# Optimization experiments

Hardware: AMD Instinct MI355X
Metric: run time of the kernel (lower is better)

The kernel has to match this reference:

```python
import jax, jax.numpy as jnp
import numpy as np

NUM_HEADS = 16
WINDOW = 64


def setup_inputs() -> dict:
    key = jax.random.key(0)
    ks = jax.random.split(key, 6)
    b, l, d = 2, 2048, 1024
    s = 1.0 / np.sqrt(d)
    return {
        "x": jax.random.normal(ks[0], (b, l, d), dtype=jnp.float32),
        "Wq": jax.random.normal(ks[1], (d, d), dtype=jnp.float32) * s,
        "Wk": jax.random.normal(ks[2], (d, d), dtype=jnp.float32) * s,
        "Wv": jax.random.normal(ks[3], (d, d), dtype=jnp.float32) * s,
        "Wo": jax.random.normal(ks[4], (d, d), dtype=jnp.float32) * s,
        "bo": jax.random.normal(ks[5], (d,), dtype=jnp.float32) * 0.01,
    }


def reference(x, Wq, Wk, Wv, Wo, bo):
    b, l, d = x.shape
    h, w = NUM_HEADS, WINDOW
    dh = d // h
    p = w // 2
    # Projections. Padding is zeros and proj_k/proj_v have no bias, so
    # padding-then-projecting equals projecting-then-zero-padding.
    q = (x @ Wq.T).reshape(b, l, h, dh)                     # (b,l,h,dh)
    xp = jnp.pad(x, ((0, 0), (p, p), (0, 0)))               # (b,l+2p,d)
    k = (xp @ Wk.T).reshape(b, l + 2 * p, h, dh)
    v = (xp @ Wv.T).reshape(b, l + 2 * p, h, dh)
    # Sliding windows: query i attends to padded positions i .. i+w-1
    win_idx = jnp.arange(l)[:, None] + jnp.arange(w)[None, :]  # (l,w)
    kw = k[:, win_idx]                                       # (b,l,w,h,dh)
    vw = v[:, win_idx]                                       # (b,l,w,h,dh)
    scale = 1.0 / np.float32(np.sqrt(dh))
    scores = jnp.einsum('blhd,blwhd->blhw', q, kw) * scale   # (b,l,h,w)
    attn = jax.nn.softmax(scores, axis=-1)
    out = jnp.einsum('blhw,blwhd->blhd', attn, vw).reshape(b, l, d)
    return out @ Wo.T + bo
```

## Files before the change

kernel.cpp:

```cpp
#include <hip/hip_runtime.h>
#include <hip/hip_bf16.h>
#include <cstdint>

typedef __bf16 bf16;
typedef __bf16 bf16x4 __attribute__((ext_vector_type(4)));
typedef __bf16 bf16x8 __attribute__((ext_vector_type(8)));
typedef float floatx4 __attribute__((ext_vector_type(4)));

typedef __attribute__((address_space(1))) void as1_void;
typedef __attribute__((address_space(3))) void as3_void;

__device__ __forceinline__ void gld16(const void* g, void* l) {
#if __has_builtin(__builtin_amdgcn_global_load_lds)
  __builtin_amdgcn_global_load_lds((as1_void*)(uintptr_t)g, (as3_void*)l, 16, 0, 0);
#else
  *(uint4*)l = *(const uint4*)g;
#endif
}

__global__ __launch_bounds__(256) void convert_kernel(
    const float* __restrict__ x, const float* __restrict__ wq,
    const float* __restrict__ wk, const float* __restrict__ wv,
    const float* __restrict__ wo, bf16* __restrict__ xbf,
    bf16* __restrict__ wqkv, bf16* __restrict__ wob) {
  int i = blockIdx.x * 256 + threadIdx.x;
  const float* src;
  bf16* dst;
  int off;
  if (i < 1048576) {
    src = x; dst = xbf; off = i;
  } else if (i < 1310720) {
    src = wq; dst = wqkv; off = i - 1048576;
  } else if (i < 1572864) {
    src = wk; dst = wqkv + 1048576; off = i - 1310720;
  } else if (i < 1835008) {
    src = wv; dst = wqkv + 2097152; off = i - 1572864;
  } else {
    src = wo; dst = wob; off = i - 1835008;
  }
  float4 v = ((const float4*)src)[off];
  bf16x4 o;
  o[0] = (bf16)v.x; o[1] = (bf16)v.y; o[2] = (bf16)v.z; o[3] = (bf16)v.w;
  ((bf16x4*)dst)[off] = o;
}

template <int MODE, int BN>
__global__ __launch_bounds__(256) void gemm_nt(const bf16* __restrict__ A,
                                               const bf16* __restrict__ Bm,
                                               bf16* __restrict__ Cb,
                                               float* __restrict__ Cf,
                                               const float* __restrict__ bias,
                                               int M, int N, int K) {
  constexpr int WN = BN / 2;
  constexpr int NI = WN / 16;
  __shared__ __attribute__((aligned(16))) bf16 As[128 * 32];
  __shared__ __attribute__((aligned(16))) bf16 Bs[BN * 32];
  const int tid = threadIdx.x;
  const int lane = tid & 63;
  const int wave = tid >> 6;
  const int quad = lane >> 4;
  const int n0 = lane & 15;
  const int wm = wave >> 1;
  const int wn = wave & 1;
  const int nwg = gridDim.x * gridDim.y;
  const int nid = blockIdx.y * gridDim.x + blockIdx.x;
  int sid = nid;
  if ((nwg & 7) == 0) sid = (nid & 7) * (nwg >> 3) + (nid >> 3);
  const int bN = sid % gridDim.x, bM = sid / gridDim.x;
  const bf16* Ab = A + (size_t)bM * 128 * K;
  const bf16* Bb = Bm + (size_t)bN * BN * K;
  const int c0 = tid, c1 = tid + 256;
  floatx4 acc[4][NI] = {};
  for (int k0 = 0; k0 < K; k0 += 32) {
    gld16(Ab + (size_t)(c0 >> 2) * K + k0 + (c0 & 3) * 8, &As[c0 * 8]);
    gld16(Ab + (size_t)(c1 >> 2) * K + k0 + (c1 & 3) * 8, &As[c1 * 8]);
#pragma unroll
    for (int cc = 0; cc < BN * 4; cc += 256) {
      const int c = cc + tid;
      gld16(Bb + (size_t)(c >> 2) * K + k0 + (c & 3) * 8, &Bs[c * 8]);
    }
    __syncthreads();
    bf16x8 af[4], bfr[NI];
#pragma unroll
    for (int mi = 0; mi < 4; ++mi)
      af[mi] = *(const bf16x8*)&As[(wm * 64 + mi * 16 + n0) * 32 + quad * 8];
#pragma unroll
    for (int ni = 0; ni < NI; ++ni)
      bfr[ni] = *(const bf16x8*)&Bs[(wn * WN + ni * 16 + n0) * 32 + quad * 8];
#pragma unroll
    for (int mi = 0; mi < 4; ++mi)
#pragma unroll
      for (int ni = 0; ni < NI; ++ni)
        acc[mi][ni] = __builtin_amdgcn_mfma_f32_16x16x32_bf16(
            af[mi], bfr[ni], acc[mi][ni], 0, 0, 0);
    __syncthreads();
  }
  const int rowBase = bM * 128 + wm * 64;
  const int colBase = bN * BN + wn * WN;
#pragma unroll
  for (int ni = 0; ni < NI; ++ni) {
    const int col = colBase + ni * 16 + n0;
    float badd = 0.f;
    if (MODE == 1) badd = bias[col];
#pragma unroll
    for (int mi = 0; mi < 4; ++mi)
#pragma unroll
      for (int r = 0; r < 4; ++r) {
        const int row = rowBase + mi * 16 + quad * 4 + r;
        if (MODE == 0)
          Cb[(size_t)row * N + col] = (bf16)acc[mi][ni][r];
        else
          Cf[(size_t)row * N + col] = acc[mi][ni][r] + badd;
      }
  }
}

#define BAR asm volatile("s_barrier" ::: "memory")
#define LGKM0                                         \
  do {                                                \
    asm volatile("s_waitcnt lgkmcnt(0)" ::: "memory");\
    __builtin_amdgcn_sched_barrier(0);                \
  } while (0)

#define STAGE(buf, op, h, t)                                                   \
  do {                                                                         \
    const char* g_ = ((op) ? Bb : Ab) + (size_t)(h) * 128 * Kb +               \
                     (size_t)(t) * 128 + rowOff;                               \
    char* l_ = lds + (buf) * 65536 + (op) * 32768 + (h) * 16384 + tid * 16;    \
    gld16(g_, l_);                                                             \
    gld16(g_ + 64 * Kb, l_ + 8192);                                            \
  } while (0)

#define LDA(buf, mh)                                                           \
  do {                                                                         \
    _Pragma("unroll") for (int q = 0; q < 4; ++q)                              \
      _Pragma("unroll") for (int ks = 0; ks < 2; ++ks)                         \
        aR[q][ks] = *(const bf16x8*)(lds + (buf) * 65536 + wm * 16384 +        \
            ((mh) * 64 + q * 16 + n0) * 128 + ((ks * 64 + quad * 16) ^ swz));  \
  } while (0)

#define LDB(buf, g)                                                            \
  do {                                                                         \
    _Pragma("unroll") for (int j = 0; j < 2; ++j)                              \
      _Pragma("unroll") for (int ks = 0; ks < 2; ++ks) {                       \
        const int row_ = wn * 64 + ((g) * 2 + j) * 16 + n0;                    \
        bR[g][j][ks] = *(const bf16x8*)(lds + (buf) * 65536 + 32768 +          \
            (row_ >> 7) * 16384 + (row_ & 127) * 128 +                         \
            ((ks * 64 + quad * 16) ^ swz));                                    \
      }                                                                        \
  } while (0)

#define MM(mh, nh)                                                             \
  do {                                                                         \
    __builtin_amdgcn_s_setprio(1);                                             \
    _Pragma("unroll") for (int q = 0; q < 4; ++q)                              \
      _Pragma("unroll") for (int j = 0; j < 2; ++j)                            \
        _Pragma("unroll") for (int ks = 0; ks < 2; ++ks)                       \
          acc[(mh) * 4 + q][(nh) * 2 + j] =                                    \
              __builtin_amdgcn_mfma_f32_16x16x32_bf16(                         \
                  aR[q][ks], bR[nh][j][ks],                                    \
                  acc[(mh) * 4 + q][(nh) * 2 + j], 0, 0, 0);                   \
    __builtin_amdgcn_s_setprio(0);                                             \
  } while (0)

__global__ __launch_bounds__(512, 2) void gemm256_nt(
    const bf16* __restrict__ A, const bf16* __restrict__ Bm,
    bf16* __restrict__ C, int M, int N, int K) {
  __shared__ __attribute__((aligned(16))) char lds[131072];
  const int tid = threadIdx.x;
  const int lane = tid & 63, wave = tid >> 6;
  const int quad = lane >> 4, n0 = lane & 15;
  const int wm = wave >> 2, wn = wave & 3;
  const int swz = (n0 & 7) << 4;
  const size_t Kb = (size_t)K * 2;
  const char* Ab = (const char*)(A + (size_t)blockIdx.y * 256 * K);
  const char* Bb = (const char*)(Bm + (size_t)blockIdx.x * 256 * K);
  const int srow = tid >> 3;
  const size_t rowOff = (size_t)srow * Kb + (size_t)(16 * ((tid & 7) ^ (srow & 7)));

  floatx4 acc[8][4] = {};
  bf16x8 aR[4][2];
  bf16x8 bR[2][2][2];

  const int NT = K >> 6;
  const int NI = K >> 7;

  STAGE(0, 0, 0, 0); STAGE(0, 0, 1, 0); STAGE(0, 1, 0, 0); STAGE(0, 1, 1, 0);
  STAGE(1, 1, 0, 1); STAGE(1, 0, 0, 1);
  asm volatile("s_waitcnt vmcnt(4)" ::: "memory");
  BAR;

  for (int i = 0; i < NI; ++i) {
    const int T = 2 * i;
    const bool s2 = (T + 2 < NT), s3 = (T + 3 < NT);
    LDB(0, 0); LDA(0, 0);
    STAGE(1, 0, 1, T + 1);
    BAR; LGKM0; MM(0, 0); BAR;
    LDB(0, 1);
    STAGE(1, 1, 1, T + 1);
    BAR; LGKM0; MM(0, 1); BAR;
    LDA(0, 1);
    if (s2) STAGE(0, 1, 0, T + 2);
    BAR; LGKM0; MM(1, 0); BAR;
    if (s2) STAGE(0, 1, 1, T + 2);
    BAR; MM(1, 1);
    if (i + 1 < NI) { asm volatile("s_waitcnt vmcnt(4)" ::: "memory"); }
    else           { asm volatile("s_waitcnt vmcnt(0)" ::: "memory"); }
    BAR;
    LDB(1, 0); LDA(1, 0);
    if (s2) STAGE(0, 0, 0, T + 2);
    BAR; LGKM0; MM(0, 0); BAR;
    LDB(1, 1);
    if (s2) STAGE(0, 0, 1, T + 2);
    BAR; LGKM0; MM(0, 1); BAR;
    LDA(1, 1);
    if (s3) STAGE(1, 1, 0, T + 3);
    BAR; LGKM0; MM(1, 0); BAR;
    if (s3) STAGE(1, 0, 0, T + 3);
    BAR; MM(1, 1);
    asm volatile("s_waitcnt vmcnt(4)" ::: "memory");
    BAR;
  }

  const int rowBase = blockIdx.y * 256 + wm * 128 + quad * 4;
  const int colBase = blockIdx.x * 256 + wn * 64 + n0;
#pragma unroll
  for (int mi = 0; mi < 8; ++mi)
#pragma unroll
    for (int ni = 0; ni < 4; ++ni)
#pragma unroll
      for (int r = 0; r < 4; ++r)
        C[(size_t)(rowBase + mi * 16 + r) * N + colBase + ni * 16] =
            (bf16)acc[mi][ni][r];
}

#undef BAR
#undef LGKM0
#undef STAGE
#undef LDA
#undef LDB
#undef MM

__global__ __launch_bounds__(256) void attn_kernel(const bf16* __restrict__ qkv,
                                                   bf16* __restrict__ aout) {
  __shared__ __attribute__((aligned(16))) bf16 Ks[128 * 72];
  __shared__ __attribute__((aligned(16))) bf16 VsPs[128 * 72];
  __shared__ __attribute__((aligned(16))) bf16 Vt[64 * 136];
  const int bid = blockIdx.x;
  const int b = bid >> 9;
  const int h = (bid >> 5) & 15;
  const int i0 = (bid & 31) * 64;
  const int tid = threadIdx.x;
  const int wave = tid >> 6, lane = tid & 63;
  const int quad = lane >> 4, n0 = lane & 15;
  bf16* Vs = VsPs;

  bf16x8 aq[2];
#pragma unroll
  for (int ks = 0; ks < 2; ++ks)
    aq[ks] = *(const bf16x8*)(qkv +
        (size_t)(b * 2048 + i0 + wave * 16 + n0) * 3072 + h * 64 + ks * 32 + quad * 8);

#pragma unroll
  for (int it = 0; it < 4; ++it) {
    const int idx = it * 256 + tid;
    const int r = idx >> 3, c = idx & 7;
    const int j = i0 - 32 + r;
    uint4 kv_ = make_uint4(0u, 0u, 0u, 0u);
    uint4 vv = make_uint4(0u, 0u, 0u, 0u);
    if (j >= 0 && j < 2048) {
      const bf16* base = qkv + (size_t)(b * 2048 + j) * 3072 + 1024 + h * 64 + c * 8;
      kv_ = *(const uint4*)base;
      vv = *(const uint4*)(base + 1024);
    }
    *(uint4*)&Ks[r * 72 + c * 8] = kv_;
    *(uint4*)&Vs[r * 72 + c * 8] = vv;
  }
  __syncthreads();

#pragma unroll
  for (int it = 0; it < 4; ++it) {
    const int idx = it * 256 + tid;
    const int t = idx & 127, c = idx >> 7;
    bf16x8 v = *(const bf16x8*)&Vs[t * 72 + c * 8];
#pragma unroll
    for (int jj = 0; jj < 8; ++jj) Vt[(c * 8 + jj) * 136 + t] = v[jj];
  }
  __syncthreads();

  floatx4 accS[8] = {};
#pragma unroll
  for (int nt = 0; nt < 8; ++nt)
#pragma unroll
    for (int ks = 0; ks < 2; ++ks) {
      bf16x8 bk = *(const bf16x8*)&Ks[(nt * 16 + n0) * 72 + ks * 32 + quad * 8];
      accS[nt] = __builtin_amdgcn_mfma_f32_16x16x32_bf16(aq[ks], bk, accS[nt], 0, 0, 0);
    }

  float mrow[4] = {-1e30f, -1e30f, -1e30f, -1e30f};
#pragma unroll
  for (int nt = 0; nt < 8; ++nt)
#pragma unroll
    for (int r = 0; r < 4; ++r) {
      const int q64 = wave * 16 + quad * 4 + r;
      const int t = nt * 16 + n0;
      float s = accS[nt][r] * 0.125f;
      if (t < q64 || t >= q64 + 64) s = -1e30f;
      accS[nt][r] = s;
      mrow[r] = fmaxf(mrow[r], s);
    }
#pragma unroll
  for (int off = 1; off < 16; off <<= 1)
#pragma unroll
    for (int r = 0; r < 4; ++r)
      mrow[r] = fmaxf(mrow[r], __shfl_xor(mrow[r], off));
  float lrow[4] = {0.f, 0.f, 0.f, 0.f};
#pragma unroll
  for (int nt = 0; nt < 8; ++nt)
#pragma unroll
    for (int r = 0; r < 4; ++r) {
      const float e = __expf(accS[nt][r] - mrow[r]);
      accS[nt][r] = e;
      lrow[r] += e;
    }
#pragma unroll
  for (int off = 1; off < 16; off <<= 1)
#pragma unroll
    for (int r = 0; r < 4; ++r) lrow[r] += __shfl_xor(lrow[r], off);

  bf16* Pw = &VsPs[wave * 16 * 136];
#pragma unroll
  for (int r = 0; r < 4; ++r) {
    const float inv = 1.f / lrow[r];
#pragma unroll
    for (int nt = 0; nt < 8; ++nt)
      Pw[(quad * 4 + r) * 136 + nt * 16 + n0] = (bf16)(accS[nt][r] * inv);
  }

  floatx4 accO[4] = {};
#pragma unroll
  for (int kt = 0; kt < 4; ++kt) {
    bf16x8 ap = *(const bf16x8*)&Pw[n0 * 136 + kt * 32 + quad * 8];
#pragma unroll
    for (int dt = 0; dt < 4; ++dt) {
      bf16x8 bv = *(const bf16x8*)&Vt[(dt * 16 + n0) * 136 + kt * 32 + quad * 8];
      accO[dt] = __builtin_amdgcn_mfma_f32_16x16x32_bf16(ap, bv, accO[dt], 0, 0, 0);
    }
  }
#pragma unroll
  for (int dt = 0; dt < 4; ++dt)
#pragma unroll
    for (int r = 0; r < 4; ++r) {
      const int q64 = wave * 16 + quad * 4 + r;
      aout[(size_t)(b * 2048 + i0 + q64) * 1024 + h * 64 + dt * 16 + n0] =
          (bf16)accO[dt][r];
    }
}

extern "C" void kernel_launch(void* const* d_in, const int* in_sizes, int n_in,
                              void* d_out, int out_size, void* d_ws, size_t ws_size,
                              hipStream_t stream) {
  const float* x = (const float*)d_in[0];
  const float* wq = (const float*)d_in[1];
  const float* wk = (const float*)d_in[2];
  const float* wv = (const float*)d_in[3];
  const float* wo = (const float*)d_in[4];
  const float* bo = (const float*)d_in[5];
  char* ws = (char*)d_ws;
  bf16* xbf = (bf16*)(ws);
  bf16* wqkv = (bf16*)(ws + (8u << 20));
  bf16* wob = (bf16*)(ws + (14u << 20));
  bf16* qkv = (bf16*)(ws + (16u << 20));
  bf16* aout = xbf;

  convert_kernel<<<8192, 256, 0, stream>>>(x, wq, wk, wv, wo, xbf, wqkv, wob);
  gemm256_nt<<<dim3(12, 16), 512, 0, stream>>>(xbf, wqkv, qkv, 4096, 3072, 1024);
  attn_kernel<<<1024, 256, 0, stream>>>(qkv, aout);
  gemm_nt<1, 64><<<dim3(16, 32), 256, 0, stream>>>(aout, wob, nullptr,
                                                   (float*)d_out, bo, 4096, 1024,
                                                   1024);
}
```

Measured before the change: 154.5 us.

## Use 256x192 tiles in QKV GEMM to fill all CUs

The QKV projection GEMM tile changes from 256x256 to 256x192, so the grid grows from 192 to 256 blocks, one per CU on a 256-CU part, and the tail wave goes away. The LDS staging, fragment loads, MFMA groups and vmcnt waits are reworked to match the uneven 3-column B split per wave and the smaller LDS footprint. In exchange, arithmetic intensity per block drops and the pipeline schedule is less symmetric.

Result: faster. 151.3 us (-2.1%).

```diff
diff --git a/kernel.cpp b/kernel.cpp
--- a/kernel.cpp
+++ b/kernel.cpp
@@ -122,51 +122,56 @@
     __builtin_amdgcn_sched_barrier(0);                \
   } while (0)
 
-#define STAGE(buf, op, h, t)                                                   \
-  do {                                                                         \
-    const char* g_ = ((op) ? Bb : Ab) + (size_t)(h) * 128 * Kb +               \
-                     (size_t)(t) * 128 + rowOff;                               \
-    char* l_ = lds + (buf) * 65536 + (op) * 32768 + (h) * 16384 + tid * 16;    \
-    gld16(g_, l_);                                                             \
-    gld16(g_ + 64 * Kb, l_ + 8192);                                            \
-  } while (0)
-
-#define LDA(buf, mh)                                                           \
+#define STAGEU(buf, op, u, t)                                                  \
+  gld16(((op) ? Bb : Ab) + (size_t)(u) * 64 * Kb + (size_t)(t) * 128 + rowOff, \
+        lds + (buf) * 57344 + (op) * 32768 + (u) * 8192 + tid * 16)
+
+#define LDA_(buf, mh)                                                          \
   do {                                                                         \
     _Pragma("unroll") for (int q = 0; q < 4; ++q)                              \
       _Pragma("unroll") for (int ks = 0; ks < 2; ++ks)                         \
-        aR[q][ks] = *(const bf16x8*)(lds + (buf) * 65536 + wm * 16384 +        \
-            ((mh) * 64 + q * 16 + n0) * 128 + ((ks * 64 + quad * 16) ^ swz));  \
-  } while (0)
-
-#define LDB(buf, g)                                                            \
+        aR[q][ks] = *(const bf16x8*)(lds + (buf) * 57344 +                     \
+            (wm * 2 + (mh)) * 8192 + (q * 16 + n0) * 128 +                     \
+            ((ks * 64 + quad * 16) ^ swz));                                    \
+  } while (0)
+
+#define LDB_(buf, g)                                                           \
   do {                                                                         \
-    _Pragma("unroll") for (int j = 0; j < 2; ++j)                              \
+    _Pragma("unroll") for (int j = 0; j < ((g) ? 1 : 2); ++j)                  \
       _Pragma("unroll") for (int ks = 0; ks < 2; ++ks) {                       \
-        const int row_ = wn * 64 + ((g) * 2 + j) * 16 + n0;                    \
-        bR[g][j][ks] = *(const bf16x8*)(lds + (buf) * 65536 + 32768 +          \
-            (row_ >> 7) * 16384 + (row_ & 127) * 128 +                         \
+        const int ni_ = (g) ? 2 : j;                                           \
+        const int row_ = wn * 48 + ni_ * 16 + n0;                              \
+        bR[ni_][ks] = *(const bf16x8*)(lds + (buf) * 57344 + 32768 +           \
+            (row_ >> 6) * 8192 + (row_ & 63) * 128 +                           \
             ((ks * 64 + quad * 16) ^ swz));                                    \
       }                                                                        \
   } while (0)
 
-#define MM(mh, nh)                                                             \
+#define MMg0(mh)                                                               \
   do {                                                                         \
     __builtin_amdgcn_s_setprio(1);                                             \
     _Pragma("unroll") for (int q = 0; q < 4; ++q)                              \
       _Pragma("unroll") for (int j = 0; j < 2; ++j)                            \
         _Pragma("unroll") for (int ks = 0; ks < 2; ++ks)                       \
-          acc[(mh) * 4 + q][(nh) * 2 + j] =                                    \
-              __builtin_amdgcn_mfma_f32_16x16x32_bf16(                         \
-                  aR[q][ks], bR[nh][j][ks],                                    \
-                  acc[(mh) * 4 + q][(nh) * 2 + j], 0, 0, 0);                   \
+          acc[(mh) * 4 + q][j] = __builtin_amdgcn_mfma_f32_16x16x32_bf16(      \
+              aR[q][ks], bR[j][ks], acc[(mh) * 4 + q][j], 0, 0, 0);            \
     __builtin_amdgcn_s_setprio(0);                                             \
   } while (0)
 
-__global__ __launch_bounds__(512, 2) void gemm256_nt(
+#define MMg1(mh)                                                               \
+  do {                                                                         \
+    __builtin_amdgcn_s_setprio(1);                                             \
+    _Pragma("unroll") for (int q = 0; q < 4; ++q)                              \
+      _Pragma("unroll") for (int ks = 0; ks < 2; ++ks)                         \
+        acc[(mh) * 4 + q][2] = __builtin_amdgcn_mfma_f32_16x16x32_bf16(        \
+            aR[q][ks], bR[2][ks], acc[(mh) * 4 + q][2], 0, 0, 0);              \
+    __builtin_amdgcn_s_setprio(0);                                             \
+  } while (0)
+
+__global__ __launch_bounds__(512, 2) void gemm192_nt(
     const bf16* __restrict__ A, const bf16* __restrict__ Bm,
     bf16* __restrict__ C, int M, int N, int K) {
-  __shared__ __attribute__((aligned(16))) char lds[131072];
+  __shared__ __attribute__((aligned(16))) char lds[114688];
   const int tid = threadIdx.x;
   const int lane = tid & 63, wave = tid >> 6;
   const int quad = lane >> 4, n0 = lane & 15;
@@ -174,60 +179,63 @@
   const int swz = (n0 & 7) << 4;
   const size_t Kb = (size_t)K * 2;
   const char* Ab = (const char*)(A + (size_t)blockIdx.y * 256 * K);
-  const char* Bb = (const char*)(Bm + (size_t)blockIdx.x * 256 * K);
+  const char* Bb = (const char*)(Bm + (size_t)blockIdx.x * 192 * K);
   const int srow = tid >> 3;
   const size_t rowOff = (size_t)srow * Kb + (size_t)(16 * ((tid & 7) ^ (srow & 7)));
 
-  floatx4 acc[8][4] = {};
+  floatx4 acc[8][3] = {};
   bf16x8 aR[4][2];
-  bf16x8 bR[2][2][2];
+  bf16x8 bR[3][2];
 
   const int NT = K >> 6;
   const int NI = K >> 7;
 
-  STAGE(0, 0, 0, 0); STAGE(0, 0, 1, 0); STAGE(0, 1, 0, 0); STAGE(0, 1, 1, 0);
-  STAGE(1, 1, 0, 1); STAGE(1, 0, 0, 1);
-  asm volatile("s_waitcnt vmcnt(4)" ::: "memory");
+  STAGEU(0, 0, 0, 0); STAGEU(0, 0, 1, 0); STAGEU(0, 0, 2, 0); STAGEU(0, 0, 3, 0);
+  STAGEU(0, 1, 0, 0); STAGEU(0, 1, 1, 0); STAGEU(0, 1, 2, 0);
+  STAGEU(1, 1, 0, 1); STAGEU(1, 1, 1, 1); STAGEU(1, 1, 2, 1);
+  STAGEU(1, 0, 0, 1); STAGEU(1, 0, 2, 1);
+  asm volatile("s_waitcnt vmcnt(5)" ::: "memory");
   BAR;
 
   for (int i = 0; i < NI; ++i) {
     const int T = 2 * i;
-    const bool s2 = (T + 2 < NT), s3 = (T + 3 < NT);
-    LDB(0, 0); LDA(0, 0);
-    STAGE(1, 0, 1, T + 1);
-    BAR; LGKM0; MM(0, 0); BAR;
-    LDB(0, 1);
-    STAGE(1, 1, 1, T + 1);
-    BAR; LGKM0; MM(0, 1); BAR;
-    LDA(0, 1);
-    if (s2) STAGE(0, 1, 0, T + 2);
-    BAR; LGKM0; MM(1, 0); BAR;
-    if (s2) STAGE(0, 1, 1, T + 2);
-    BAR; MM(1, 1);
-    if (i + 1 < NI) { asm volatile("s_waitcnt vmcnt(4)" ::: "memory"); }
-    else           { asm volatile("s_waitcnt vmcnt(0)" ::: "memory"); }
+    const bool s2 = (T + 2 < NT);
+    LDB_(0, 0); LDA_(0, 0);
+    STAGEU(1, 0, 1, T + 1);
+    BAR; LGKM0; MMg0(0); BAR;
+    LDB_(0, 1);
+    STAGEU(1, 0, 3, T + 1);
+    BAR; LGKM0; MMg1(0); BAR;
+    LDA_(0, 1);
+    if (s2) { STAGEU(0, 1, 0, T + 2); STAGEU(0, 1, 1, T + 2); }
+    BAR; LGKM0; MMg0(1); BAR;
+    if (s2) STAGEU(0, 1, 2, T + 2);
+    BAR; MMg1(1);
+    if (i + 1 < NI) { asm volatile("s_waitcnt vmcnt(3)" ::: "memory"); }
+    else            { asm volatile("s_waitcnt vmcnt(0)" ::: "memory"); }
     BAR;
-    LDB(1, 0); LDA(1, 0);
-    if (s2) STAGE(0, 0, 0, T + 2);
-    BAR; LGKM0; MM(0, 0); BAR;
-    LDB(1, 1);
-    if (s2) STAGE(0, 0, 1, T + 2);
-    BAR; LGKM0; MM(0, 1); BAR;
-    LDA(1, 1);
-    if (s3) STAGE(1, 1, 0, T + 3);
-    BAR; LGKM0; MM(1, 0); BAR;
-    if (s3) STAGE(1, 0, 0, T + 3);
-    BAR; MM(1, 1);
-    asm volatile("s_waitcnt vmcnt(4)" ::: "memory");
+    LDB_(1, 0); LDA_(1, 0);
+    if (s2) { STAGEU(0, 0, 0, T + 2); STAGEU(0, 0, 2, T + 2); }
+    BAR; LGKM0; MMg0(0); BAR;
+    LDB_(1, 1);
+    if (s2) STAGEU(0, 0, 1, T + 2);
+    BAR; LGKM0; MMg1(0); BAR;
+    LDA_(1, 1);
+    if (s2) { STAGEU(0, 0, 3, T + 2); STAGEU(1, 1, 0, T + 3); }
+    BAR; LGKM0; MMg0(1); BAR;
+    if (s2) { STAGEU(1, 1, 1, T + 3); STAGEU(1, 1, 2, T + 3);
+              STAGEU(1, 0, 0, T + 3); STAGEU(1, 0, 2, T + 3); }
+    BAR; MMg1(1);
+    asm volatile("s_waitcnt vmcnt(5)" ::: "memory");
     BAR;
   }
 
   const int rowBase = blockIdx.y * 256 + wm * 128 + quad * 4;
-  const int colBase = blockIdx.x * 256 + wn * 64 + n0;
+  const int colBase = blockIdx.x * 192 + wn * 48 + n0;
 #pragma unroll
   for (int mi = 0; mi < 8; ++mi)
 #pragma unroll
-    for (int ni = 0; ni < 4; ++ni)
+    for (int ni = 0; ni < 3; ++ni)
 #pragma unroll
       for (int r = 0; r < 4; ++r)
         C[(size_t)(rowBase + mi * 16 + r) * N + colBase + ni * 16] =
@@ -236,10 +244,11 @@
 
 #undef BAR
 #undef LGKM0
-#undef STAGE
-#undef LDA
-#undef LDB
-#undef MM
+#undef STAGEU
+#undef LDA_
+#undef LDB_
+#undef MMg0
+#undef MMg1
 
 __global__ __launch_bounds__(256) void attn_kernel(const bf16* __restrict__ qkv,
                                                    bf16* __restrict__ aout) {
@@ -374,7 +383,7 @@
   bf16* aout = xbf;
 
   convert_kernel<<<8192, 256, 0, stream>>>(x, wq, wk, wv, wo, xbf, wqkv, wob);
-  gemm256_nt<<<dim3(12, 16), 512, 0, stream>>>(xbf, wqkv, qkv, 4096, 3072, 1024);
+  gemm192_nt<<<dim3(16, 16), 512, 0, stream>>>(xbf, wqkv, qkv, 4096, 3072, 1024);
   attn_kernel<<<1024, 256, 0, stream>>>(qkv, aout);
   gemm_nt<1, 64><<<dim3(16, 32), 256, 0, stream>>>(aout, wob, nullptr,
                                                    (float*)d_out, bo, 4096, 1024,
```
